# Kernel optimization log

Measured on AMD Instinct MI355X. Metric: run time of the kernel, lower is better.

## Reference

```python
import jax, jax.numpy as jnp
import numpy as np

VOCAB = 50257
SEQ = 2048
EMB = 512
BATCH = 8


def setup_inputs() -> dict:
    key = jax.random.key(0)
    k1, k2, k3 = jax.random.split(key, 3)
    tokens = jax.random.randint(k1, (BATCH, SEQ), 0, VOCAB, dtype=jnp.int64 if jax.config.jax_enable_x64 else jnp.int32)
    W_emb = jax.random.normal(k2, (EMB, VOCAB), dtype=jnp.float32)
    W_pos = jax.random.normal(k3, (SEQ, EMB), dtype=jnp.float32)
    return {"tokens": tokens, "W_emb": W_emb, "W_pos": W_pos}


def reference(tokens, W_emb, W_pos):
    # Original: one_hot(tokens, V).float() @ W_emb.T  -> identical to gathering
    # columns of W_emb, i.e. rows of W_emb.T. Shapes: (B,S) -> (B,S,E)
    tok_emb = jnp.take(W_emb.T, tokens, axis=0)  # (B, S, E)
    # positional weight (S, E) broadcasts over batch
    return tok_emb + W_pos
```

## Files before the change

kernel.cpp:

```cpp
#include <hip/hip_runtime.h>

#define VOCAB 50257
#define SEQ   2048
#define EMB   512
#define BATCH 8
#define NTOK  (BATCH * SEQ)

typedef float floatx2 __attribute__((ext_vector_type(2)));


__global__ __launch_bounds__(256)
void slab_scatter_k(const int* __restrict__ tokens,
                    const float* __restrict__ W,
                    const floatx2* __restrict__ Wpos2,
                    floatx2* __restrict__ out2) {
    __shared__ float slab[64][129];

    const int v0   = blockIdx.x * 64;
    const int eoff = blockIdx.y * 128;
    const int tid  = threadIdx.x;
    const int lane = tid & 63;
    const int wv   = tid >> 6;
    const int v    = v0 + lane;

    if (v < VOCAB) {
        const float* rp = W + (size_t)(eoff + wv) * VOCAB + v;
        const int cbase = (wv & 1) * 64 + (wv >> 1);
#pragma unroll
        for (int j = 0; j < 32; ++j) {
            slab[lane][cbase + 2 * j] = rp[(size_t)(4 * j) * VOCAB];
        }
    }
    __syncthreads();

    const int wbase = wv * (NTOK / 4);
    const int ecol2 = (eoff >> 1) + lane;
#pragma unroll 4
    for (int k = 0; k < (NTOK / 4) / 64; ++k) {
        const int i = wbase + k * 64 + lane;
        const unsigned d = (unsigned)(tokens[i] - v0);
        unsigned long long mask = __ballot(d < 64u);
        while (mask) {
            const int b = (int)__builtin_ctzll(mask);
            mask &= mask - 1;
            const int p  = wbase + k * 64 + b;
            const int vl = __shfl((int)d, b);
            const int s  = p & (SEQ - 1);
            const float* wrow = slab[vl];
            const floatx2 wp = Wpos2[(size_t)s * (EMB / 2) + ecol2];
            floatx2 r;
            r.x = wrow[lane];
            r.y = wrow[64 + lane];
            __builtin_nontemporal_store(
                r + wp, &out2[(size_t)p * (EMB / 2) + ecol2]);
        }
    }
}

extern "C" void kernel_launch(void* const* d_in, const int* in_sizes, int n_in,
                              void* d_out, int out_size, void* d_ws, size_t ws_size,
                              hipStream_t stream) {
    const int*   tokens = (const int*)d_in[0];
    const float* W_emb  = (const float*)d_in[1];
    const float* W_pos  = (const float*)d_in[2];
    float*       out    = (float*)d_out;

    (void)d_ws; (void)ws_size;

    slab_scatter_k<<<dim3((VOCAB + 63) / 64, EMB / 128), 256, 0, stream>>>(
        tokens, W_emb, (const floatx2*)W_pos, (floatx2*)out);
}
```

Before: 219.9 us.

## Build per-token linked lists so slab blocks visit only their own positions

Two small pre-kernels are added. One resets a head array in workspace, and the other uses atomicExch to build a linked list of token positions for each vocabulary id. The slab kernel then walks only the lists for the vocab ids it owns, instead of every block scanning all 16K tokens with ballots. This removes the redundant full token scan repeated across about 3,000 blocks, in exchange for two extra launches and serial pointer-chasing inside each list. A direct gather kernel serves as a fallback when the workspace is too small.

After: 177.1 us. 1.24x faster.

```diff
diff --git a/kernel.cpp b/kernel.cpp
--- a/kernel.cpp
+++ b/kernel.cpp
@@ -9,12 +9,33 @@
 typedef float floatx2 __attribute__((ext_vector_type(2)));
 
 
+#define HEAD_OFF 0
+#define NEXT_OFF 50432
+#define WS_INTS  (NEXT_OFF + NTOK)
+
 __global__ __launch_bounds__(256)
-void slab_scatter_k(const int* __restrict__ tokens,
+void init_head_k(int* __restrict__ head) {
+    const int i = blockIdx.x * 256 + threadIdx.x;
+    if (i < VOCAB) head[i] = -1;
+}
+
+__global__ __launch_bounds__(256)
+void links_k(const int* __restrict__ tokens, int* __restrict__ head,
+             int* __restrict__ next) {
+    const int i = blockIdx.x * 256 + threadIdx.x;
+    next[i] = atomicExch(&head[tokens[i]], i);
+}
+
+__global__ __launch_bounds__(256)
+void slab_scatter_k(const int* __restrict__ head,
+                    const int* __restrict__ next,
                     const float* __restrict__ W,
                     const floatx2* __restrict__ Wpos2,
                     floatx2* __restrict__ out2) {
     __shared__ float slab[64][129];
+    __shared__ int   u_vl[64];
+    __shared__ int   u_hd[64];
+    __shared__ int   nused_s;
 
     const int v0   = blockIdx.x * 64;
     const int eoff = blockIdx.y * 128;
@@ -22,6 +43,14 @@
     const int lane = tid & 63;
     const int wv   = tid >> 6;
     const int v    = v0 + lane;
+
+    if (tid < 64) {
+        const int h = (v < VOCAB) ? head[v] : -1;
+        const unsigned long long m = __ballot(h >= 0);
+        const int pos = __popcll(m & ((1ull << lane) - 1ull));
+        if (h >= 0) { u_vl[pos] = lane; u_hd[pos] = h; }
+        if (lane == 0) nused_s = (int)__popcll(m);
+    }
 
     if (v < VOCAB) {
         const float* rp = W + (size_t)(eoff + wv) * VOCAB + v;
@@ -33,28 +62,42 @@
     }
     __syncthreads();
 
-    const int wbase = wv * (NTOK / 4);
+    const int nused = nused_s;
     const int ecol2 = (eoff >> 1) + lane;
-#pragma unroll 4
-    for (int k = 0; k < (NTOK / 4) / 64; ++k) {
-        const int i = wbase + k * 64 + lane;
-        const unsigned d = (unsigned)(tokens[i] - v0);
-        unsigned long long mask = __ballot(d < 64u);
-        while (mask) {
-            const int b = (int)__builtin_ctzll(mask);
-            mask &= mask - 1;
-            const int p  = wbase + k * 64 + b;
-            const int vl = __shfl((int)d, b);
-            const int s  = p & (SEQ - 1);
-            const float* wrow = slab[vl];
-            const floatx2 wp = Wpos2[(size_t)s * (EMB / 2) + ecol2];
-            floatx2 r;
-            r.x = wrow[lane];
-            r.y = wrow[64 + lane];
+    for (int u = wv; u < nused; u += 4) {
+        const int vl = u_vl[u];
+        int p = u_hd[u];
+        floatx2 col;
+        col.x = slab[vl][lane];
+        col.y = slab[vl][64 + lane];
+        while (p >= 0) {
+            const int s = p & (SEQ - 1);
+            const floatx2 r = col + Wpos2[(size_t)s * (EMB / 2) + ecol2];
             __builtin_nontemporal_store(
-                r + wp, &out2[(size_t)p * (EMB / 2) + ecol2]);
+                r, &out2[(size_t)p * (EMB / 2) + ecol2]);
+            p = next[p];
         }
     }
+}
+
+typedef float floatx4 __attribute__((ext_vector_type(4)));
+__global__ __launch_bounds__(256)
+void gather_direct_k(const int* __restrict__ tokens,
+                     const float* __restrict__ W_emb,
+                     const floatx4* __restrict__ Wpos,
+                     floatx4* __restrict__ out) {
+    const int idx = blockIdx.x * blockDim.x + threadIdx.x;
+    const int e4  = idx & (EMB / 4 - 1);
+    const int ts  = idx >> 7;
+    const int s   = ts & (SEQ - 1);
+    const int t   = tokens[ts];
+    const size_t base = (size_t)(4 * e4) * VOCAB + (size_t)t;
+    floatx4 r;
+    r.x = W_emb[base];
+    r.y = W_emb[base + (size_t)VOCAB];
+    r.z = W_emb[base + (size_t)(2 * VOCAB)];
+    r.w = W_emb[base + (size_t)(3 * VOCAB)];
+    __builtin_nontemporal_store(r + Wpos[(size_t)s * (EMB / 4) + e4], &out[idx]);
 }
 
 extern "C" void kernel_launch(void* const* d_in, const int* in_sizes, int n_in,
@@ -65,8 +108,19 @@
     const float* W_pos  = (const float*)d_in[2];
     float*       out    = (float*)d_out;
 
-    (void)d_ws; (void)ws_size;
+    const size_t need = (size_t)WS_INTS * sizeof(int);
+    if (ws_size >= need) {
+        int* head = (int*)d_ws + HEAD_OFF;
+        int* next = (int*)d_ws + NEXT_OFF;
 
-    slab_scatter_k<<<dim3((VOCAB + 63) / 64, EMB / 128), 256, 0, stream>>>(
-        tokens, W_emb, (const floatx2*)W_pos, (floatx2*)out);
+        init_head_k<<<(VOCAB + 255) / 256, 256, 0, stream>>>(head);
+        links_k<<<NTOK / 256, 256, 0, stream>>>(tokens, head, next);
+        slab_scatter_k<<<dim3((VOCAB + 63) / 64, EMB / 128), 256, 0, stream>>>(
+            head, next, W_emb, (const floatx2*)W_pos, (floatx2*)out);
+    } else {
+        const int gblocks = BATCH * SEQ * (EMB / 4) / 256;
+        gather_direct_k<<<gblocks, 256, 0, stream>>>(tokens, W_emb,
+                                                     (const floatx4*)W_pos,
+                                                     (floatx4*)out);
+    }
 }
```
